# Optimization experiments

Hardware: AMD Instinct MI355X
Metric: run time of the kernel (lower is better)

## Reference

```python
import jax, jax.numpy as jnp
import numpy as np

L, H, P = 16384, 256, 512


def setup_inputs() -> dict:
    key = jax.random.key(0)
    ks = jax.random.split(key, 7)
    return {
        "input_sequence": jax.random.normal(ks[0], (L, H), jnp.float32),
        "A_diag": jax.random.normal(ks[1], (P,), jnp.float32) * 2.0,
        "G_diag": jax.random.uniform(ks[2], (P,), jnp.float32),  # in [0,1): keeps 1 - sigmoid(dt)*G > 0
        "dt": jax.random.normal(ks[3], (P,), jnp.float32) * 0.5,
        "B": jax.random.uniform(ks[4], (P, H, 2), jnp.float32, -1.0, 1.0) / np.sqrt(H).astype(np.float32),
        "C": jax.random.uniform(ks[5], (H, P, 2), jnp.float32, -1.0, 1.0) / np.sqrt(P).astype(np.float32),
        "D": jax.random.normal(ks[6], (H,), jnp.float32),
    }


def _combine(q_i, q_j):
    # q = (A, b); A: (..., 4, P) real 2x2 block-diagonal entries [A,B,C,D], b: (..., 2, P) complex
    A_i, b_i = q_i
    A_j, b_j = q_j
    iA, iB, iC, iD = A_i[..., 0, :], A_i[..., 1, :], A_i[..., 2, :], A_i[..., 3, :]
    jA, jB, jC, jD = A_j[..., 0, :], A_j[..., 1, :], A_j[..., 2, :], A_j[..., 3, :]
    A_new = jnp.stack(
        [jA * iA + jB * iC, jA * iB + jB * iD, jC * iA + jD * iC, jC * iB + jD * iD],
        axis=-2,
    )
    b1, b2 = b_i[..., 0, :], b_i[..., 1, :]
    b_new = jnp.stack([jA * b1 + jB * b2, jC * b1 + jD * b2], axis=-2) + b_j
    return (A_new, b_new)


def reference(input_sequence, A_diag, G_diag, dt, B, C, D):
    # complex parameter assembly
    B_c = B[..., 0] + 1j * B[..., 1]      # (P, H) complex
    C_c = C[..., 0] + 1j * C[..., 1]      # (H, P) complex

    # _soft_project_AGdt
    dts = jax.nn.sigmoid(dt)
    G = jax.nn.relu(G_diag)
    root = jnp.sqrt(1.0 - dts * G)
    denom = jnp.maximum(dts ** 2, 1e-6)
    A_low = (2.0 - dts * G - 2.0 * root) / denom
    A_high = (2.0 - dts * G + 2.0 * root) / denom
    A = A_low + jax.nn.relu(A_diag - A_low) - jax.nn.relu(A_diag - A_high)

    # Bu_k = B_complex @ u_k for all k: (L, P) complex64
    Bu = input_sequence.astype(B_c.dtype) @ B_c.T

    # IMEX2 transition matrix (diagonal 2x2 blocks), constant over time
    M = jnp.stack(
        [1.0 - dts * G, -dts * A, dts * (1.0 - dts * G), 1.0 - dts ** 2 * A],
        axis=0,
    )  # (4, P)
    seq_len = input_sequence.shape[0]
    M_el = jnp.broadcast_to(M, (seq_len, 4, M.shape[-1]))          # (L, 4, P)
    F = jnp.stack([dts * Bu, dts ** 2 * Bu], axis=1)               # (L, 2, P) complex

    _, xs = jax.lax.associative_scan(_combine, (M_el, F))
    ys = xs[:, 1, :]                                                # x-component, (L, P) complex

    out = (ys @ C_c.T).real.astype(input_sequence.dtype) + input_sequence * D
    return out
```

## Files before the change

### kernel.cpp

```cpp
#include <hip/hip_runtime.h>
#include <math.h>

#define L_SEQ 16384
#define H_DIM 256
#define P_DIM 512
#define CL 32
#define NC (L_SEQ / CL)

typedef __attribute__((ext_vector_type(8))) short bf16x8;
typedef __attribute__((ext_vector_type(4))) float f32x4;

static __device__ __forceinline__ unsigned short f2bf(float f) {
  unsigned int u = __builtin_bit_cast(unsigned int, f);
  u += 0x7FFFu + ((u >> 16) & 1u);
  return (unsigned short)(u >> 16);
}
static __device__ __forceinline__ float bflo(unsigned int v) {
  return __builtin_bit_cast(float, v << 16);
}
static __device__ __forceinline__ float bfhi(unsigned int v) {
  return __builtin_bit_cast(float, v & 0xFFFF0000u);
}
static __device__ __forceinline__ float bf2f(unsigned short s) {
  return __builtin_bit_cast(float, (unsigned int)s << 16);
}

__global__ __launch_bounds__(256) void prep_all(
    const float* __restrict__ A_diag, const float* __restrict__ G_diag,
    const float* __restrict__ dt, const float* __restrict__ B,
    const float* __restrict__ C, const float* __restrict__ u,
    float* __restrict__ prm, unsigned short* __restrict__ W1b,
    unsigned short* __restrict__ W2b, unsigned short* __restrict__ ub) {
  const int b = blockIdx.x;
  const int t = threadIdx.x;
  if (b < 2) {
    int p = b * 256 + t;
    float dts = 1.0f / (1.0f + expf(-dt[p]));
    float G = fmaxf(G_diag[p], 0.0f);
    float g = dts * G;
    float root = sqrtf(1.0f - g);
    float denom = fmaxf(dts * dts, 1e-6f);
    float A_low  = (2.0f - g - 2.0f * root) / denom;
    float A_high = (2.0f - g + 2.0f * root) / denom;
    float Ad = A_diag[p];
    float A = A_low + fmaxf(Ad - A_low, 0.0f) - fmaxf(Ad - A_high, 0.0f);
    float m00 = 1.0f - g;
    float m01 = -dts * A;
    float m10 = dts * (1.0f - g);
    float m11 = 1.0f - dts * dts * A;
    float c00 = m00, c01 = m01, c10 = m10, c11 = m11;
#pragma unroll
    for (int i = 0; i < 5; i++) {
      float n00 = c00 * c00 + c01 * c10;
      float n01 = c00 * c01 + c01 * c11;
      float n10 = c10 * c00 + c11 * c10;
      float n11 = c10 * c01 + c11 * c11;
      c00 = n00; c01 = n01; c10 = n10; c11 = n11;
    }
    prm[0 * P_DIM + p] = m00;
    prm[1 * P_DIM + p] = m01;
    prm[2 * P_DIM + p] = m10;
    prm[3 * P_DIM + p] = m11;
    prm[4 * P_DIM + p] = dts;
    prm[5 * P_DIM + p] = dts * dts;
    prm[6 * P_DIM + p] = c00;
    prm[7 * P_DIM + p] = c01;
    prm[8 * P_DIM + p] = c10;
    prm[9 * P_DIM + p] = c11;
  } else if (b < 2 + 1024) {
    int idx = (b - 2) * 256 + t;
    int n = idx >> 8;
    int k = idx & 255;
    int p = n >> 1, c = n & 1;
    W1b[((size_t)(k >> 3) * 1024 + n) * 8 + (k & 7)] = f2bf(B[(p * H_DIM + k) * 2 + c]);
  } else if (b < 2 + 2048) {
    int idx = (b - 1026) * 256 + t;
    int h = idx >> 10;
    int k = idx & 1023;
    int p = k >> 1, c = k & 1;
    float v = C[(h * P_DIM + p) * 2 + c];
    W2b[((size_t)(k >> 3) * 256 + h) * 8 + (k & 7)] = f2bf(c ? -v : v);
  } else {
    int idx = (b - 2050) * 256 + t;
    float4 v = ((const float4*)u)[idx];
    ushort4 o;
    o.x = f2bf(v.x); o.y = f2bf(v.y); o.z = f2bf(v.z); o.w = f2bf(v.w);
    ((ushort4*)ub)[idx] = o;
  }
}

__global__ __launch_bounds__(256) void gemm1_scan(
    const unsigned short* __restrict__ A, const unsigned short* __restrict__ W,
    unsigned short* __restrict__ Out,
    const float* __restrict__ prm, float4* __restrict__ finals) {
  constexpr int N = 1024, K = H_DIM;
  __shared__ unsigned short tA[128 * 32];
  __shared__ unsigned short tW[128 * 32];
  __shared__ unsigned short stg[128 * 132];
  const int tid = threadIdx.x;
  const int lane = tid & 63;
  const int wid = tid >> 6;
  const int wr = wid >> 1;
  const int wc = wid & 1;
  const int bm = blockIdx.x * 128;
  const int bn = blockIdx.y * 128;

  f32x4 acc[4][4] = {};
  const int rA = lane & 15;
  const int g = lane >> 4;

  for (int k0 = 0; k0 < K; k0 += 32) {
    __syncthreads();
#pragma unroll
    for (int c = wid; c < 8; c += 4) {
      const int unit = c * 64 + lane;
      const int kg = unit >> 7, r = unit & 127;
      const unsigned short* src = A + ((size_t)(bm + r) * 32 + (k0 >> 3) + kg) * 8;
      __builtin_amdgcn_global_load_lds(
          (const __attribute__((address_space(1))) void*)src,
          (__attribute__((address_space(3))) void*)(tA + c * 512), 16, 0, 0);
    }
#pragma unroll
    for (int c = wid; c < 8; c += 4) {
      const int unit = c * 64 + lane;
      const int kg = unit >> 7, n = unit & 127;
      const unsigned short* src = W + ((size_t)((k0 >> 3) + kg) * 1024 + bn + n) * 8;
      __builtin_amdgcn_global_load_lds(
          (const __attribute__((address_space(1))) void*)src,
          (__attribute__((address_space(3))) void*)(tW + c * 512), 16, 0, 0);
    }
    __syncthreads();

    bf16x8 af[4], wf[4];
#pragma unroll
    for (int i = 0; i < 4; i++)
      af[i] = *(const bf16x8*)&tA[(g * 128 + wr * 64 + i * 16 + rA) * 8];
#pragma unroll
    for (int j = 0; j < 4; j++)
      wf[j] = *(const bf16x8*)&tW[(g * 128 + wc * 64 + j * 16 + rA) * 8];
#pragma unroll
    for (int i = 0; i < 4; i++)
#pragma unroll
      for (int j = 0; j < 4; j++)
        acc[i][j] = __builtin_amdgcn_mfma_f32_16x16x32_bf16(af[i], wf[j], acc[i][j], 0, 0, 0);
  }

  const int cr = (lane >> 4) * 4;
  const int cc = lane & 15;
#pragma unroll
  for (int i = 0; i < 4; i++)
#pragma unroll
    for (int j = 0; j < 4; j++) {
      const int rl = wr * 64 + i * 16 + cr;
      const int clc = wc * 64 + j * 16 + cc;
#pragma unroll
      for (int q = 0; q < 4; q++) {
        const unsigned short hv = f2bf(acc[i][j][q]);
        Out[(size_t)(bm + rl + q) * N + bn + clc] = hv;
        stg[(rl + q) * 132 + clc] = hv;
      }
    }

  __syncthreads();
  {
    const int i = tid >> 6;
    const int pl = tid & 63;
    const int p = (bn >> 1) + pl;
    const int cglob = blockIdx.x * 4 + i;
    float m00 = prm[0 * P_DIM + p], m01 = prm[1 * P_DIM + p];
    float m10 = prm[2 * P_DIM + p], m11 = prm[3 * P_DIM + p];
    float dts = prm[4 * P_DIM + p], dts2 = prm[5 * P_DIM + p];
    float x1r = 0.f, x2r = 0.f, x1i = 0.f, x2i = 0.f;
    const unsigned int* stg32 = (const unsigned int*)stg;
#pragma unroll 8
    for (int s = 0; s < CL; s++) {
      unsigned int v = stg32[(i * 32 + s) * 66 + pl];
      float bx = bflo(v), by = bfhi(v);
      float n1r = fmaf(m00, x1r, fmaf(m01, x2r, dts * bx));
      float n2r = fmaf(m10, x1r, fmaf(m11, x2r, dts2 * bx));
      float n1i = fmaf(m00, x1i, fmaf(m01, x2i, dts * by));
      float n2i = fmaf(m10, x1i, fmaf(m11, x2i, dts2 * by));
      x1r = n1r; x2r = n2r; x1i = n1i; x2i = n2i;
    }
    finals[(size_t)cglob * P_DIM + p] = make_float4(x1r, x2r, x1i, x2i);
  }
}

__global__ __launch_bounds__(NC) void scan_carry(
    const float4* __restrict__ finals, const float* __restrict__ prm,
    float4* __restrict__ carry) {
  int p = blockIdx.x;
  int c = threadIdx.x;
  __shared__ float4 sb[NC];
  float m00 = prm[6 * P_DIM + p], m01 = prm[7 * P_DIM + p];
  float m10 = prm[8 * P_DIM + p], m11 = prm[9 * P_DIM + p];
  float4 b = finals[c * P_DIM + p];
  for (int o = 1; o < NC; o <<= 1) {
    sb[c] = b;
    __syncthreads();
    float4 nb = (c >= o) ? sb[c - o] : make_float4(0.f, 0.f, 0.f, 0.f);
    __syncthreads();
    b.x = fmaf(m00, nb.x, fmaf(m01, nb.y, b.x));
    b.y = fmaf(m10, nb.x, fmaf(m11, nb.y, b.y));
    b.z = fmaf(m00, nb.z, fmaf(m01, nb.w, b.z));
    b.w = fmaf(m10, nb.z, fmaf(m11, nb.w, b.w));
    float n00 = m00 * m00 + m01 * m10;
    float n01 = m00 * m01 + m01 * m11;
    float n10 = m10 * m00 + m11 * m10;
    float n11 = m10 * m01 + m11 * m11;
    m00 = n00; m01 = n01; m10 = n10; m11 = n11;
  }
  if (c + 1 < NC) carry[(c + 1) * P_DIM + p] = b;
  if (c == 0) carry[p] = make_float4(0.f, 0.f, 0.f, 0.f);
}

__global__ __launch_bounds__(256) void gemm2_fused(
    const unsigned int* __restrict__ Bu16, const float* __restrict__ prm,
    const float4* __restrict__ carry, const unsigned short* __restrict__ W2b,
    const unsigned short* __restrict__ ub, const float* __restrict__ Dv,
    float* __restrict__ out) {
  __shared__ unsigned int yA[32 * 512];
  const int tid = threadIdx.x;
  const int lane = tid & 63;
  const int wid = tid >> 6;
  const int row0 = blockIdx.x * 32;

#pragma unroll
  for (int h = 0; h < 2; h++) {
    const int p = tid + h * 256;
    float m00 = prm[0 * P_DIM + p], m01 = prm[1 * P_DIM + p];
    float m10 = prm[2 * P_DIM + p], m11 = prm[3 * P_DIM + p];
    float dts = prm[4 * P_DIM + p], dts2 = prm[5 * P_DIM + p];
    float4 s = carry[(size_t)blockIdx.x * P_DIM + p];
    float x1r = s.x, x2r = s.y, x1i = s.z, x2i = s.w;
    const unsigned int* src = Bu16 + (size_t)row0 * P_DIM + p;
#pragma unroll 8
    for (int i = 0; i < 32; i++) {
      unsigned int v = src[(size_t)i * P_DIM];
      float bx = bflo(v), by = bfhi(v);
      float n1r = fmaf(m00, x1r, fmaf(m01, x2r, dts * bx));
      float n2r = fmaf(m10, x1r, fmaf(m11, x2r, dts2 * bx));
      float n1i = fmaf(m00, x1i, fmaf(m01, x2i, dts * by));
      float n2i = fmaf(m10, x1i, fmaf(m11, x2i, dts2 * by));
      yA[(i * 512 + p) ^ ((i & 7) << 2)] =
          (unsigned int)f2bf(n2r) | ((unsigned int)f2bf(n2i) << 16);
      x1r = n1r; x2r = n2r; x1i = n1i; x2i = n2i;
    }
  }
  __syncthreads();

  const int wr = wid >> 1;
  const int wc = wid & 1;
  const int rA = lane & 15;
  const int g = lane >> 4;
  const int arow = wr * 16 + rA;
  const unsigned short* yAs = (const unsigned short*)yA;
  const unsigned short* wbase = W2b + ((size_t)g * 256 + wc * 128 + rA) * 8;
  f32x4 acc[8] = {};

#pragma unroll 4
  for (int t = 0; t < 32; t++) {
    bf16x8 af = *(const bf16x8*)&yAs[((unsigned)(arow * 1024 + t * 32 + g * 8)) ^ ((arow & 7) << 3)];
#pragma unroll
    for (int j = 0; j < 8; j++) {
      bf16x8 wf = *(const bf16x8*)&wbase[(size_t)t * 8192 + j * 128];
      acc[j] = __builtin_amdgcn_mfma_f32_16x16x32_bf16(af, wf, acc[j], 0, 0, 0);
    }
  }

  const int cr = (lane >> 4) * 4;
  const int cc = lane & 15;
#pragma unroll
  for (int j = 0; j < 8; j++) {
    const int col = wc * 128 + j * 16 + cc;
    const float d = Dv[col];
#pragma unroll
    for (int q = 0; q < 4; q++) {
      const int row = row0 + wr * 16 + cr + q;
      const size_t idx = (size_t)row * H_DIM + col;
      out[idx] = fmaf(bf2f(ub[idx]), d, acc[j][q]);
    }
  }
}

extern "C" void kernel_launch(void* const* d_in, const int* in_sizes, int n_in,
                              void* d_out, int out_size, void* d_ws, size_t ws_size,
                              hipStream_t stream) {
  const float* u      = (const float*)d_in[0];
  const float* A_diag = (const float*)d_in[1];
  const float* G_diag = (const float*)d_in[2];
  const float* dt     = (const float*)d_in[3];
  const float* B      = (const float*)d_in[4];
  const float* C      = (const float*)d_in[5];
  const float* D      = (const float*)d_in[6];
  float* out = (float*)d_out;

  char* w = (char*)d_ws;
  unsigned short* Bu16 = (unsigned short*)w;
  unsigned short* ub   = (unsigned short*)(w + (size_t)L_SEQ * 1024 * 2);
  unsigned short* W1b  = ub + (size_t)L_SEQ * H_DIM;
  unsigned short* W2b  = W1b + 1024 * H_DIM;
  float* prm    = (float*)(W2b + H_DIM * 1024);
  float* finals = prm + 8192;
  float* carryb = finals + (size_t)NC * P_DIM * 4;

  prep_all<<<2 + 1024 + 1024 + 4096, 256, 0, stream>>>(
      A_diag, G_diag, dt, B, C, u, prm, W1b, W2b, ub);

  gemm1_scan<<<dim3(L_SEQ / 128, 1024 / 128), 256, 0, stream>>>(
      ub, W1b, Bu16, prm, (float4*)finals);

  scan_carry<<<P_DIM, NC, 0, stream>>>(
      (const float4*)finals, prm, (float4*)carryb);

  gemm2_fused<<<L_SEQ / 32, 256, 0, stream>>>(
      (const unsigned int*)Bu16, prm, (const float4*)carryb, W2b, ub, D, out);
}
```

Before: 79.99 us.

## Split-K the second GEMM with atomic accumulation and precompute skip term

The output GEMM now uses 128-row tiles with the P dimension split across four blocks. Each block recomputes its slice of the chunk scan and accumulates partial results into the output with float atomicAdd. The D*u skip term is written to the output in the prep kernel, using full-precision u instead of the bf16 copy. This aims to raise reuse of W2 per block and shrink the per-block scan work, at the cost of many global atomics and a 4x larger atomic write volume.

```diff
diff --git a/kernel.cpp b/kernel.cpp
--- a/kernel.cpp
+++ b/kernel.cpp
@@ -21,16 +21,15 @@
 static __device__ __forceinline__ float bfhi(unsigned int v) {
   return __builtin_bit_cast(float, v & 0xFFFF0000u);
 }
-static __device__ __forceinline__ float bf2f(unsigned short s) {
-  return __builtin_bit_cast(float, (unsigned int)s << 16);
-}
 
 __global__ __launch_bounds__(256) void prep_all(
     const float* __restrict__ A_diag, const float* __restrict__ G_diag,
     const float* __restrict__ dt, const float* __restrict__ B,
     const float* __restrict__ C, const float* __restrict__ u,
+    const float* __restrict__ Dv,
     float* __restrict__ prm, unsigned short* __restrict__ W1b,
-    unsigned short* __restrict__ W2b, unsigned short* __restrict__ ub) {
+    unsigned short* __restrict__ W2b, unsigned short* __restrict__ ub,
+    float* __restrict__ out) {
   const int b = blockIdx.x;
   const int t = threadIdx.x;
   if (b < 2) {
@@ -86,6 +85,10 @@
     ushort4 o;
     o.x = f2bf(v.x); o.y = f2bf(v.y); o.z = f2bf(v.z); o.w = f2bf(v.w);
     ((ushort4*)ub)[idx] = o;
+    const int col = (idx * 4) & (H_DIM - 1);
+    float4 d = *(const float4*)(Dv + col);
+    float4 ov = make_float4(v.x * d.x, v.y * d.y, v.z * d.z, v.w * d.w);
+    ((float4*)out)[idx] = ov;
   }
 }
 
@@ -214,35 +217,40 @@
   if (c == 0) carry[p] = make_float4(0.f, 0.f, 0.f, 0.f);
 }
 
-__global__ __launch_bounds__(256) void gemm2_fused(
+__global__ __launch_bounds__(256) void gemm2_sk(
     const unsigned int* __restrict__ Bu16, const float* __restrict__ prm,
     const float4* __restrict__ carry, const unsigned short* __restrict__ W2b,
-    const unsigned short* __restrict__ ub, const float* __restrict__ Dv,
     float* __restrict__ out) {
-  __shared__ unsigned int yA[32 * 512];
+  __shared__ unsigned int yA[128 * 128];
   const int tid = threadIdx.x;
   const int lane = tid & 63;
   const int wid = tid >> 6;
-  const int row0 = blockIdx.x * 32;
+  const int row0 = blockIdx.x * 128;
+  const int ks = blockIdx.y;
+  const int p0 = ks * 128;
 
 #pragma unroll
   for (int h = 0; h < 2; h++) {
-    const int p = tid + h * 256;
+    const int idx = h * 256 + tid;
+    const int i = idx >> 7;
+    const int pl = idx & 127;
+    const int p = p0 + pl;
     float m00 = prm[0 * P_DIM + p], m01 = prm[1 * P_DIM + p];
     float m10 = prm[2 * P_DIM + p], m11 = prm[3 * P_DIM + p];
     float dts = prm[4 * P_DIM + p], dts2 = prm[5 * P_DIM + p];
-    float4 s = carry[(size_t)blockIdx.x * P_DIM + p];
+    float4 s = carry[(size_t)(blockIdx.x * 4 + i) * P_DIM + p];
     float x1r = s.x, x2r = s.y, x1i = s.z, x2i = s.w;
-    const unsigned int* src = Bu16 + (size_t)row0 * P_DIM + p;
+    const unsigned int* src = Bu16 + (size_t)(row0 + i * 32) * P_DIM + p;
 #pragma unroll 8
-    for (int i = 0; i < 32; i++) {
-      unsigned int v = src[(size_t)i * P_DIM];
+    for (int st = 0; st < 32; st++) {
+      unsigned int v = src[(size_t)st * P_DIM];
       float bx = bflo(v), by = bfhi(v);
       float n1r = fmaf(m00, x1r, fmaf(m01, x2r, dts * bx));
       float n2r = fmaf(m10, x1r, fmaf(m11, x2r, dts2 * bx));
       float n1i = fmaf(m00, x1i, fmaf(m01, x2i, dts * by));
       float n2i = fmaf(m10, x1i, fmaf(m11, x2i, dts2 * by));
-      yA[(i * 512 + p) ^ ((i & 7) << 2)] =
+      const int row = i * 32 + st;
+      yA[(row * 128 + pl) ^ ((row & 7) << 2)] =
           (unsigned int)f2bf(n2r) | ((unsigned int)f2bf(n2i) << 16);
       x1r = n1r; x2r = n2r; x1i = n1i; x2i = n2i;
     }
@@ -253,34 +261,39 @@
   const int wc = wid & 1;
   const int rA = lane & 15;
   const int g = lane >> 4;
-  const int arow = wr * 16 + rA;
   const unsigned short* yAs = (const unsigned short*)yA;
-  const unsigned short* wbase = W2b + ((size_t)g * 256 + wc * 128 + rA) * 8;
-  f32x4 acc[8] = {};
-
-#pragma unroll 4
-  for (int t = 0; t < 32; t++) {
-    bf16x8 af = *(const bf16x8*)&yAs[((unsigned)(arow * 1024 + t * 32 + g * 8)) ^ ((arow & 7) << 3)];
+  const unsigned short* wbase = W2b + (((size_t)ks * 32 + g) * 256 + wc * 128 + rA) * 8;
+  f32x4 acc[4][8] = {};
+
+#pragma unroll 2
+  for (int t = 0; t < 8; t++) {
+    bf16x8 af[4];
+#pragma unroll
+    for (int m = 0; m < 4; m++) {
+      const int r = wr * 64 + m * 16 + rA;
+      af[m] = *(const bf16x8*)&yAs[((unsigned)(r * 256 + t * 32 + g * 8)) ^ ((r & 7) << 3)];
+    }
 #pragma unroll
     for (int j = 0; j < 8; j++) {
       bf16x8 wf = *(const bf16x8*)&wbase[(size_t)t * 8192 + j * 128];
-      acc[j] = __builtin_amdgcn_mfma_f32_16x16x32_bf16(af, wf, acc[j], 0, 0, 0);
+#pragma unroll
+      for (int m = 0; m < 4; m++)
+        acc[m][j] = __builtin_amdgcn_mfma_f32_16x16x32_bf16(af[m], wf, acc[m][j], 0, 0, 0);
     }
   }
 
   const int cr = (lane >> 4) * 4;
   const int cc = lane & 15;
 #pragma unroll
-  for (int j = 0; j < 8; j++) {
-    const int col = wc * 128 + j * 16 + cc;
-    const float d = Dv[col];
-#pragma unroll
-    for (int q = 0; q < 4; q++) {
-      const int row = row0 + wr * 16 + cr + q;
-      const size_t idx = (size_t)row * H_DIM + col;
-      out[idx] = fmaf(bf2f(ub[idx]), d, acc[j][q]);
-    }
-  }
+  for (int m = 0; m < 4; m++)
+#pragma unroll
+    for (int j = 0; j < 8; j++) {
+      const int rowg = row0 + wr * 64 + m * 16 + cr;
+      const int col = wc * 128 + j * 16 + cc;
+#pragma unroll
+      for (int q = 0; q < 4; q++)
+        atomicAdd(&out[(size_t)(rowg + q) * H_DIM + col], acc[m][j][q]);
+    }
 }
 
 extern "C" void kernel_launch(void* const* d_in, const int* in_sizes, int n_in,
@@ -305,7 +318,7 @@
   float* carryb = finals + (size_t)NC * P_DIM * 4;
 
   prep_all<<<2 + 1024 + 1024 + 4096, 256, 0, stream>>>(
-      A_diag, G_diag, dt, B, C, u, prm, W1b, W2b, ub);
+      A_diag, G_diag, dt, B, C, u, D, prm, W1b, W2b, ub, out);
 
   gemm1_scan<<<dim3(L_SEQ / 128, 1024 / 128), 256, 0, stream>>>(
       ub, W1b, Bu16, prm, (float4*)finals);
@@ -313,6 +326,6 @@
   scan_carry<<<P_DIM, NC, 0, stream>>>(
       (const float4*)finals, prm, (float4*)carryb);
 
-  gemm2_fused<<<L_SEQ / 32, 256, 0, stream>>>(
-      (const unsigned int*)Bu16, prm, (const float4*)carryb, W2b, ub, D, out);
-}
+  gemm2_sk<<<dim3(L_SEQ / 128, 4), 256, 0, stream>>>(
+      (const unsigned int*)Bu16, prm, (const float4*)carryb, W2b, out);
+}
```

After: 113.7 us. 42.1% more time.

## Store local scan outputs in gemm1 and apply carry correction separately

Applied to the files above, without the earlier changes.

The first GEMM kernel now writes the per-chunk local scan outputs (x2 component) directly instead of the raw Bu values. A new elementwise kernel adds the carry contribution using precomputed powers of the transition matrix (aT, bT rows for each step within a chunk). The second GEMM becomes a lean double-buffered tiled GEMM using global_load_lds, no longer re-running the sequential scan. This removes the serial recurrence from gemm2 but adds an extra launch and a full read-modify-write pass over the ys buffer, with an extra bf16 rounding of ys before the correction.

```diff
diff --git a/kernel.cpp b/kernel.cpp
--- a/kernel.cpp
+++ b/kernel.cpp
@@ -24,13 +24,17 @@
 static __device__ __forceinline__ float bf2f(unsigned short s) {
   return __builtin_bit_cast(float, (unsigned int)s << 16);
 }
+static __device__ __forceinline__ unsigned int pack2(float r, float i) {
+  return (unsigned int)f2bf(r) | ((unsigned int)f2bf(i) << 16);
+}
 
 __global__ __launch_bounds__(256) void prep_all(
     const float* __restrict__ A_diag, const float* __restrict__ G_diag,
     const float* __restrict__ dt, const float* __restrict__ B,
     const float* __restrict__ C, const float* __restrict__ u,
     float* __restrict__ prm, unsigned short* __restrict__ W1b,
-    unsigned short* __restrict__ W2b, unsigned short* __restrict__ ub) {
+    unsigned short* __restrict__ W2b, unsigned short* __restrict__ ub,
+    float* __restrict__ aT, float* __restrict__ bT) {
   const int b = blockIdx.x;
   const int t = threadIdx.x;
   if (b < 2) {
@@ -48,6 +52,16 @@
     float m01 = -dts * A;
     float m10 = dts * (1.0f - g);
     float m11 = 1.0f - dts * dts * A;
+    float e00 = m00, e01 = m01, e10 = m10, e11 = m11;
+    for (int s = 0; s < 32; s++) {
+      aT[s * P_DIM + p] = e10;
+      bT[s * P_DIM + p] = e11;
+      float f00 = m00 * e00 + m01 * e10;
+      float f01 = m00 * e01 + m01 * e11;
+      float f10 = m10 * e00 + m11 * e10;
+      float f11 = m10 * e01 + m11 * e11;
+      e00 = f00; e01 = f01; e10 = f10; e11 = f11;
+    }
     float c00 = m00, c01 = m01, c10 = m10, c11 = m11;
 #pragma unroll
     for (int i = 0; i < 5; i++) {
@@ -91,9 +105,9 @@
 
 __global__ __launch_bounds__(256) void gemm1_scan(
     const unsigned short* __restrict__ A, const unsigned short* __restrict__ W,
-    unsigned short* __restrict__ Out,
+    unsigned int* __restrict__ ys,
     const float* __restrict__ prm, float4* __restrict__ finals) {
-  constexpr int N = 1024, K = H_DIM;
+  constexpr int K = H_DIM;
   __shared__ unsigned short tA[128 * 32];
   __shared__ unsigned short tW[128 * 32];
   __shared__ unsigned short stg[128 * 132];
@@ -154,11 +168,8 @@
       const int rl = wr * 64 + i * 16 + cr;
       const int clc = wc * 64 + j * 16 + cc;
 #pragma unroll
-      for (int q = 0; q < 4; q++) {
-        const unsigned short hv = f2bf(acc[i][j][q]);
-        Out[(size_t)(bm + rl + q) * N + bn + clc] = hv;
-        stg[(rl + q) * 132 + clc] = hv;
-      }
+      for (int q = 0; q < 4; q++)
+        stg[(rl + q) * 132 + clc] = f2bf(acc[i][j][q]);
     }
 
   __syncthreads();
@@ -172,6 +183,7 @@
     float dts = prm[4 * P_DIM + p], dts2 = prm[5 * P_DIM + p];
     float x1r = 0.f, x2r = 0.f, x1i = 0.f, x2i = 0.f;
     const unsigned int* stg32 = (const unsigned int*)stg;
+    unsigned int* dst = ys + (size_t)(bm + i * 32) * P_DIM + p;
 #pragma unroll 8
     for (int s = 0; s < CL; s++) {
       unsigned int v = stg32[(i * 32 + s) * 66 + pl];
@@ -180,6 +192,7 @@
       float n2r = fmaf(m10, x1r, fmaf(m11, x2r, dts2 * bx));
       float n1i = fmaf(m00, x1i, fmaf(m01, x2i, dts * by));
       float n2i = fmaf(m10, x1i, fmaf(m11, x2i, dts2 * by));
+      dst[(size_t)s * P_DIM] = pack2(n2r, n2i);
       x1r = n1r; x2r = n2r; x1i = n1i; x2i = n2i;
     }
     finals[(size_t)cglob * P_DIM + p] = make_float4(x1r, x2r, x1i, x2i);
@@ -214,73 +227,104 @@
   if (c == 0) carry[p] = make_float4(0.f, 0.f, 0.f, 0.f);
 }
 
-__global__ __launch_bounds__(256) void gemm2_fused(
-    const unsigned int* __restrict__ Bu16, const float* __restrict__ prm,
-    const float4* __restrict__ carry, const unsigned short* __restrict__ W2b,
+__global__ __launch_bounds__(256) void correct_ys(
+    unsigned int* __restrict__ ys, const float4* __restrict__ carry,
+    const float* __restrict__ aT, const float* __restrict__ bT) {
+  const int i4 = blockIdx.x * 256 + threadIdx.x;
+  const int tg = i4 >> 7;
+  const int p0 = (i4 & 127) * 4;
+  const int c = tg >> 5, t = tg & 31;
+  uint4 v = ((const uint4*)ys)[i4];
+  const float4 a = *(const float4*)&aT[t * P_DIM + p0];
+  const float4 b = *(const float4*)&bT[t * P_DIM + p0];
+  const float4* cb = carry + (size_t)c * P_DIM + p0;
+  float4 x0 = cb[0], x1 = cb[1], x2 = cb[2], x3 = cb[3];
+  v.x = pack2(bflo(v.x) + a.x * x0.x + b.x * x0.y, bfhi(v.x) + a.x * x0.z + b.x * x0.w);
+  v.y = pack2(bflo(v.y) + a.y * x1.x + b.y * x1.y, bfhi(v.y) + a.y * x1.z + b.y * x1.w);
+  v.z = pack2(bflo(v.z) + a.z * x2.x + b.z * x2.y, bfhi(v.z) + a.z * x2.z + b.z * x2.w);
+  v.w = pack2(bflo(v.w) + a.w * x3.x + b.w * x3.y, bfhi(v.w) + a.w * x3.z + b.w * x3.w);
+  ((uint4*)ys)[i4] = v;
+}
+
+__global__ __launch_bounds__(256) void gemm2_lean(
+    const unsigned short* __restrict__ ys16, const unsigned short* __restrict__ W2b,
     const unsigned short* __restrict__ ub, const float* __restrict__ Dv,
     float* __restrict__ out) {
-  __shared__ unsigned int yA[32 * 512];
+  __shared__ unsigned short tA[2][64 * 32];
+  __shared__ unsigned short tW[2][128 * 32];
   const int tid = threadIdx.x;
   const int lane = tid & 63;
   const int wid = tid >> 6;
-  const int row0 = blockIdx.x * 32;
-
-#pragma unroll
-  for (int h = 0; h < 2; h++) {
-    const int p = tid + h * 256;
-    float m00 = prm[0 * P_DIM + p], m01 = prm[1 * P_DIM + p];
-    float m10 = prm[2 * P_DIM + p], m11 = prm[3 * P_DIM + p];
-    float dts = prm[4 * P_DIM + p], dts2 = prm[5 * P_DIM + p];
-    float4 s = carry[(size_t)blockIdx.x * P_DIM + p];
-    float x1r = s.x, x2r = s.y, x1i = s.z, x2i = s.w;
-    const unsigned int* src = Bu16 + (size_t)row0 * P_DIM + p;
-#pragma unroll 8
-    for (int i = 0; i < 32; i++) {
-      unsigned int v = src[(size_t)i * P_DIM];
-      float bx = bflo(v), by = bfhi(v);
-      float n1r = fmaf(m00, x1r, fmaf(m01, x2r, dts * bx));
-      float n2r = fmaf(m10, x1r, fmaf(m11, x2r, dts2 * bx));
-      float n1i = fmaf(m00, x1i, fmaf(m01, x2i, dts * by));
-      float n2i = fmaf(m10, x1i, fmaf(m11, x2i, dts2 * by));
-      yA[(i * 512 + p) ^ ((i & 7) << 2)] =
-          (unsigned int)f2bf(n2r) | ((unsigned int)f2bf(n2i) << 16);
-      x1r = n1r; x2r = n2r; x1i = n1i; x2i = n2i;
-    }
-  }
-  __syncthreads();
-
+  const int bm = blockIdx.x * 64;
+  const int bn = blockIdx.y * 128;
+
+  const int rA = lane & 15;
+  const int g = lane >> 4;
   const int wr = wid >> 1;
   const int wc = wid & 1;
-  const int rA = lane & 15;
-  const int g = lane >> 4;
-  const int arow = wr * 16 + rA;
-  const unsigned short* yAs = (const unsigned short*)yA;
-  const unsigned short* wbase = W2b + ((size_t)g * 256 + wc * 128 + rA) * 8;
-  f32x4 acc[8] = {};
-
-#pragma unroll 4
+
+  const int a_row = (wid * 64 + lane) >> 2;
+  const int a_sd = (wid * 64 + lane) & 3;
+  const int a_ss = a_sd ^ ((a_row >> 1) & 3);
+
+  auto STAGE = [&](int buf, int k0) {
+    {
+      const unsigned short* src = ys16 + (size_t)(bm + a_row) * 1024 + k0 + a_ss * 8;
+      __builtin_amdgcn_global_load_lds(
+          (const __attribute__((address_space(1))) void*)src,
+          (__attribute__((address_space(3))) void*)(&tA[buf][wid * 512]), 16, 0, 0);
+    }
+#pragma unroll
+    for (int c = wid; c < 8; c += 4) {
+      const int unit = c * 64 + lane;
+      const int kg = unit >> 7, n = unit & 127;
+      const unsigned short* src = W2b + (((size_t)(k0 >> 3) + kg) * 256 + bn + n) * 8;
+      __builtin_amdgcn_global_load_lds(
+          (const __attribute__((address_space(1))) void*)src,
+          (__attribute__((address_space(3))) void*)(&tW[buf][c * 512]), 16, 0, 0);
+    }
+  };
+
+  f32x4 acc[2][4] = {};
+  STAGE(0, 0);
+  __syncthreads();
+
   for (int t = 0; t < 32; t++) {
-    bf16x8 af = *(const bf16x8*)&yAs[((unsigned)(arow * 1024 + t * 32 + g * 8)) ^ ((arow & 7) << 3)];
-#pragma unroll
-    for (int j = 0; j < 8; j++) {
-      bf16x8 wf = *(const bf16x8*)&wbase[(size_t)t * 8192 + j * 128];
-      acc[j] = __builtin_amdgcn_mfma_f32_16x16x32_bf16(af, wf, acc[j], 0, 0, 0);
-    }
+    const int cur = t & 1;
+    if (t < 31) STAGE(cur ^ 1, (t + 1) * 32);
+    bf16x8 af[2], wf[4];
+#pragma unroll
+    for (int m = 0; m < 2; m++) {
+      const int r = wr * 32 + m * 16 + rA;
+      const int unit = r * 4 + (g ^ ((r >> 1) & 3));
+      af[m] = *(const bf16x8*)&tA[cur][unit * 8];
+    }
+#pragma unroll
+    for (int j = 0; j < 4; j++)
+      wf[j] = *(const bf16x8*)&tW[cur][(g * 128 + wc * 64 + j * 16 + rA) * 8];
+#pragma unroll
+    for (int m = 0; m < 2; m++)
+#pragma unroll
+      for (int j = 0; j < 4; j++)
+        acc[m][j] = __builtin_amdgcn_mfma_f32_16x16x32_bf16(af[m], wf[j], acc[m][j], 0, 0, 0);
+    __syncthreads();
   }
 
   const int cr = (lane >> 4) * 4;
   const int cc = lane & 15;
 #pragma unroll
-  for (int j = 0; j < 8; j++) {
-    const int col = wc * 128 + j * 16 + cc;
-    const float d = Dv[col];
-#pragma unroll
-    for (int q = 0; q < 4; q++) {
-      const int row = row0 + wr * 16 + cr + q;
-      const size_t idx = (size_t)row * H_DIM + col;
-      out[idx] = fmaf(bf2f(ub[idx]), d, acc[j][q]);
-    }
-  }
+  for (int m = 0; m < 2; m++)
+#pragma unroll
+    for (int j = 0; j < 4; j++) {
+      const int rowg = bm + wr * 32 + m * 16 + cr;
+      const int col = bn + wc * 64 + j * 16 + cc;
+      const float d = Dv[col];
+#pragma unroll
+      for (int q = 0; q < 4; q++) {
+        const size_t idx = (size_t)(rowg + q) * H_DIM + col;
+        out[idx] = fmaf(bf2f(ub[idx]), d, acc[m][j][q]);
+      }
+    }
 }
 
 extern "C" void kernel_launch(void* const* d_in, const int* in_sizes, int n_in,
@@ -296,23 +340,28 @@
   float* out = (float*)d_out;
 
   char* w = (char*)d_ws;
-  unsigned short* Bu16 = (unsigned short*)w;
+  unsigned short* ys16 = (unsigned short*)w;
   unsigned short* ub   = (unsigned short*)(w + (size_t)L_SEQ * 1024 * 2);
   unsigned short* W1b  = ub + (size_t)L_SEQ * H_DIM;
   unsigned short* W2b  = W1b + 1024 * H_DIM;
   float* prm    = (float*)(W2b + H_DIM * 1024);
   float* finals = prm + 8192;
   float* carryb = finals + (size_t)NC * P_DIM * 4;
+  float* aT     = carryb + (size_t)NC * P_DIM * 4;
+  float* bT     = aT + 32 * P_DIM;
 
   prep_all<<<2 + 1024 + 1024 + 4096, 256, 0, stream>>>(
-      A_diag, G_diag, dt, B, C, u, prm, W1b, W2b, ub);
+      A_diag, G_diag, dt, B, C, u, prm, W1b, W2b, ub, aT, bT);
 
   gemm1_scan<<<dim3(L_SEQ / 128, 1024 / 128), 256, 0, stream>>>(
-      ub, W1b, Bu16, prm, (float4*)finals);
+      ub, W1b, (unsigned int*)ys16, prm, (float4*)finals);
 
   scan_carry<<<P_DIM, NC, 0, stream>>>(
       (const float4*)finals, prm, (float4*)carryb);
 
-  gemm2_fused<<<L_SEQ / 32, 256, 0, stream>>>(
-      (const unsigned int*)Bu16, prm, (const float4*)carryb, W2b, ub, D, out);
-}
+  correct_ys<<<(L_SEQ * P_DIM / 4) / 256, 256, 0, stream>>>(
+      (unsigned int*)ys16, (const float4*)carryb, aT, bT);
+
+  gemm2_lean<<<dim3(L_SEQ / 64, H_DIM / 128), 256, 0, stream>>>(
+      ys16, W2b, ub, D, out);
+}
```

Result: slower. 88.24 us (+10.3%).
